# Kernel optimization log

Measured on AMD Instinct MI355X. Metric: run time of the kernel, lower is better.

The kernel has to match this reference:

```python
import jax, jax.numpy as jnp
import numpy as np

N_NODES = 100000
N_EDGES = 1_600_000
N_ROIS = 400
HIDDEN = 128
N_GRAPHS = 512
OUT = 2


def setup_inputs() -> dict:
    key = jax.random.key(0)
    ks = jax.random.split(key, 7)
    x = jax.random.normal(ks[0], (N_NODES, N_ROIS), dtype=jnp.float32)
    edge_index = jax.random.randint(ks[1], (2, N_EDGES), 0, N_NODES, dtype=jnp.int32)
    # sorted graph-assignment vector; prepend arange so every graph id is non-empty
    rnd = jax.random.randint(ks[2], (N_NODES - N_GRAPHS,), 0, N_GRAPHS, dtype=jnp.int32)
    batch = jnp.sort(jnp.concatenate([jnp.arange(N_GRAPHS, dtype=jnp.int32), rnd]))
    W = jax.random.normal(ks[3], (N_ROIS, HIDDEN), dtype=jnp.float32) / np.float32(np.sqrt(N_ROIS))
    b = jnp.zeros((HIDDEN,), dtype=jnp.float32)
    lin_W = jax.random.normal(ks[4], (HIDDEN, OUT), dtype=jnp.float32) / np.float32(np.sqrt(HIDDEN))
    lin_b = jnp.zeros((OUT,), dtype=jnp.float32)
    return {"x": x, "edge_index": edge_index, "batch": batch,
            "W": W, "b": b, "lin_W": lin_W, "lin_b": lin_b}


def reference(x, edge_index, batch, W, b, lin_W, lin_b):
    N = x.shape[0]
    # GCNConv: add self-loops, symmetric normalization D^-1/2 (A+I) D^-1/2
    loops = jnp.arange(N, dtype=edge_index.dtype)
    row = jnp.concatenate([edge_index[0], loops])  # source
    col = jnp.concatenate([edge_index[1], loops])  # target
    deg = jax.ops.segment_sum(jnp.ones_like(col, dtype=x.dtype), col, num_segments=N)
    dinv = jnp.where(deg > 0, jax.lax.rsqrt(deg), 0.0)
    norm = dinv[row] * dinv[col]                   # [E+N]
    h = x @ W                                      # [N, H] transform before propagate
    msg = h[row] * norm[:, None]                   # [E+N, H]
    agg = jax.ops.segment_sum(msg, col, num_segments=N) + b
    act = jax.nn.relu(agg)                         # [N, H]
    # global max pool over graph ids (all segments guaranteed non-empty)
    pooled = jax.ops.segment_max(act, batch, num_segments=N_GRAPHS)  # [G, H]
    logits = pooled @ lin_W + lin_b                # [G, OUT]
    return logits, pooled
```

## Files before the change

kernel.cpp:

```cpp
#include <hip/hip_runtime.h>
#include <hip/hip_bf16.h>

#define N_NODES 100000
#define N_EDGES 1600000
#define N_ROIS  400
#define RKP     416
#define HID     128
#define N_GRAPHS 512
#define NOUT    2
#define NBUCK   391
#define BCAP    8192
#define ECH     4096
#define NPW     16

typedef __attribute__((ext_vector_type(8))) short short8;
typedef __attribute__((ext_vector_type(4))) float f32x4;

static __device__ __forceinline__ unsigned short f2bf(float f) {
  unsigned u = __float_as_uint(f);
  u += 0x7fffu + ((u >> 16) & 1u);
  return (unsigned short)(u >> 16);
}
static __device__ __forceinline__ float bf2f(unsigned short h) {
  return __uint_as_float(((unsigned)h) << 16);
}

__global__ __launch_bounds__(256) void bucket_k(
    const int* __restrict__ row, const int* __restrict__ col,
    int* __restrict__ bcnt, unsigned int* __restrict__ pairs) {
  __shared__ int hist[NBUCK];
  __shared__ int base[NBUCK];
  int t = threadIdx.x;
  for (int b = t; b < NBUCK; b += 256) hist[b] = 0;
  __syncthreads();
  int e0 = blockIdx.x * ECH;
  unsigned int pk[16];
  int bk[16], rk[16];
#pragma unroll
  for (int i = 0; i < 16; ++i) {
    int e = e0 + t + i * 256;
    if (e < N_EDGES) {
      int r = row[e], c = col[e];
      bk[i] = c >> 8;
      pk[i] = ((unsigned)r << 8) | (unsigned)(c & 255);
      rk[i] = atomicAdd(&hist[bk[i]], 1);
    } else bk[i] = -1;
  }
  __syncthreads();
  for (int b = t; b < NBUCK; b += 256)
    base[b] = (hist[b] > 0) ? atomicAdd(&bcnt[b], hist[b]) : 0;
  __syncthreads();
#pragma unroll
  for (int i = 0; i < 16; ++i)
    if (bk[i] >= 0) {
      int p = base[bk[i]] + rk[i];
      if (p < BCAP) pairs[(size_t)bk[i] * BCAP + p] = pk[i];
    }
}

__global__ __launch_bounds__(256) void csr_build_k(
    const unsigned int* __restrict__ pairs, const int* __restrict__ bcnt,
    int* __restrict__ csr_row, int* __restrict__ offs, int* __restrict__ cnt,
    float* __restrict__ dinv) {
  __shared__ unsigned int ep[BCAP];
  __shared__ int h[256];
  __shared__ int sc[256];
  __shared__ int cur[256];
  int b = blockIdx.x;
  int t = threadIdx.x;
  int m = min(bcnt[b], BCAP);
  size_t base = (size_t)b * BCAP;
  for (int j = t; j < m; j += 256) ep[j] = pairs[base + j];
  h[t] = 0;
  __syncthreads();
  for (int j = t; j < m; j += 256) atomicAdd(&h[ep[j] & 255u], 1);
  __syncthreads();
  int myc = h[t];
  sc[t] = myc;
  __syncthreads();
  for (int off = 1; off < 256; off <<= 1) {
    int v = (t >= off) ? sc[t - off] : 0;
    __syncthreads();
    sc[t] += v;
    __syncthreads();
  }
  int loff = sc[t] - myc;
  cur[t] = loff;
  int node = b * 256 + t;
  if (node < N_NODES) {
    cnt[node] = myc;
    offs[node] = (int)base + loff;
    dinv[node] = rsqrtf((float)(myc + 1));
  }
  __syncthreads();
  for (int j = t; j < m; j += 256) {
    unsigned int e = ep[j];
    int pos = atomicAdd(&cur[e & 255u], 1);
    csr_row[base + pos] = (int)(e >> 8);
  }
}

__global__ void prep_wt_k(const float* __restrict__ W, unsigned short* __restrict__ Wt) {
  int idx = blockIdx.x * blockDim.x + threadIdx.x;
  if (idx < HID * RKP) {
    int n = idx / RKP, k = idx - n * RKP;
    float v = (k < N_ROIS) ? W[k * HID + n] : 0.f;
    Wt[idx] = f2bf(v);
  }
}

__global__ __launch_bounds__(256) void gemm_k(
    const float* __restrict__ x, const unsigned short* __restrict__ Wt,
    const float* __restrict__ dinv, unsigned short* __restrict__ hp) {
  __shared__ __align__(16) short As[64][40];
  __shared__ __align__(16) short Bs[HID][40];
  int t = threadIdx.x;
  int lane = t & 63;
  int wv = t >> 6;
  int row0 = blockIdx.x * 64;
  int mrow = lane & 15;
  int kgrp = lane >> 4;

  f32x4 acc[8];
#pragma unroll
  for (int i = 0; i < 8; ++i) acc[i] = (f32x4){0.f, 0.f, 0.f, 0.f};

  int arow = t >> 2;
  int akofs = (t & 3) * 8;
  int brow = t >> 1;
  int bkofs = (t & 1) * 16;
  int grow_a = row0 + arow;
  const float* xp = x + (size_t)grow_a * N_ROIS;

  for (int kk = 0; kk < RKP; kk += 32) {
    short8 a8;
    if (grow_a < N_NODES && kk + akofs + 8 <= N_ROIS) {
      float4 f0 = *(const float4*)(xp + kk + akofs);
      float4 f1 = *(const float4*)(xp + kk + akofs + 4);
      a8[0] = (short)f2bf(f0.x); a8[1] = (short)f2bf(f0.y);
      a8[2] = (short)f2bf(f0.z); a8[3] = (short)f2bf(f0.w);
      a8[4] = (short)f2bf(f1.x); a8[5] = (short)f2bf(f1.y);
      a8[6] = (short)f2bf(f1.z); a8[7] = (short)f2bf(f1.w);
    } else {
#pragma unroll
      for (int u = 0; u < 8; ++u) {
        int k = kk + akofs + u;
        float f = (grow_a < N_NODES && k < N_ROIS) ? xp[k] : 0.f;
        a8[u] = (short)f2bf(f);
      }
    }
    *(short8*)&As[arow][akofs] = a8;
    const short8* wp = (const short8*)(Wt + (size_t)brow * RKP + kk + bkofs);
    *(short8*)&Bs[brow][bkofs] = wp[0];
    *(short8*)&Bs[brow][bkofs + 8] = wp[1];
    __syncthreads();

    short8 af = *(const short8*)&As[wv * 16 + mrow][kgrp * 8];
#pragma unroll
    for (int nt = 0; nt < 8; ++nt) {
      short8 bf = *(const short8*)&Bs[nt * 16 + mrow][kgrp * 8];
      acc[nt] = __builtin_amdgcn_mfma_f32_16x16x32_bf16(af, bf, acc[nt], 0, 0, 0);
    }
    __syncthreads();
  }

#pragma unroll
  for (int r = 0; r < 4; ++r) {
    int grow = row0 + wv * 16 + kgrp * 4 + r;
    if (grow < N_NODES) {
      float di = dinv[grow];
      unsigned short* op = hp + (size_t)grow * HID + mrow;
#pragma unroll
      for (int nt = 0; nt < 8; ++nt) {
        op[nt * 16] = f2bf(di * acc[nt][r]);
      }
    }
  }
}

__global__ __launch_bounds__(256) void gather_k(
    const unsigned short* __restrict__ hp, const int* __restrict__ csr_row,
    const int* __restrict__ offs, const int* __restrict__ cnt,
    const float* __restrict__ dinv, const int* __restrict__ batch,
    const float* __restrict__ bias, unsigned int* __restrict__ pooled_bits) {
  int wave = (blockIdx.x * blockDim.x + threadIdx.x) >> 6;
  int lane = threadIdx.x & 63;
  int n0 = wave * NPW;
  if (n0 >= N_NODES) return;
  int nend = min(n0 + NPW, N_NODES);
  float2 bb = *(const float2*)(bias + lane * 2);
  float rm0 = 0.f, rm1 = 0.f;
  int cur_g = batch[n0];

  for (int i = n0; i < nend; ++i) {
    int start = offs[i];
    int m = cnt[i];
    unsigned int u = *(const unsigned int*)(hp + (size_t)i * HID + lane * 2);
    float ax = bf2f((unsigned short)(u & 0xffff));
    float ay = bf2f((unsigned short)(u >> 16));
    int j = 0;
    for (; j + 4 <= m; j += 4) {
      int s0 = csr_row[start + j];
      int s1 = csr_row[start + j + 1];
      int s2 = csr_row[start + j + 2];
      int s3 = csr_row[start + j + 3];
      unsigned int u0 = *(const unsigned int*)(hp + (size_t)s0 * HID + lane * 2);
      unsigned int u1 = *(const unsigned int*)(hp + (size_t)s1 * HID + lane * 2);
      unsigned int u2 = *(const unsigned int*)(hp + (size_t)s2 * HID + lane * 2);
      unsigned int u3 = *(const unsigned int*)(hp + (size_t)s3 * HID + lane * 2);
      ax += (bf2f((unsigned short)(u0 & 0xffff)) + bf2f((unsigned short)(u1 & 0xffff)))
          + (bf2f((unsigned short)(u2 & 0xffff)) + bf2f((unsigned short)(u3 & 0xffff)));
      ay += (bf2f((unsigned short)(u0 >> 16)) + bf2f((unsigned short)(u1 >> 16)))
          + (bf2f((unsigned short)(u2 >> 16)) + bf2f((unsigned short)(u3 >> 16)));
    }
    for (; j < m; ++j) {
      int s0 = csr_row[start + j];
      unsigned int u0 = *(const unsigned int*)(hp + (size_t)s0 * HID + lane * 2);
      ax += bf2f((unsigned short)(u0 & 0xffff));
      ay += bf2f((unsigned short)(u0 >> 16));
    }
    float di = dinv[i];
    float p0 = fmaxf(fmaf(di, ax, bb.x), 0.f);
    float p1 = fmaxf(fmaf(di, ay, bb.y), 0.f);
    int g = batch[i];
    if (g != cur_g) {
      atomicMax(&pooled_bits[cur_g * HID + lane * 2],     __float_as_uint(rm0));
      atomicMax(&pooled_bits[cur_g * HID + lane * 2 + 1], __float_as_uint(rm1));
      rm0 = 0.f; rm1 = 0.f;
      cur_g = g;
    }
    rm0 = fmaxf(rm0, p0);
    rm1 = fmaxf(rm1, p1);
  }
  atomicMax(&pooled_bits[cur_g * HID + lane * 2],     __float_as_uint(rm0));
  atomicMax(&pooled_bits[cur_g * HID + lane * 2 + 1], __float_as_uint(rm1));
}

__global__ void logits_k(const float* __restrict__ pooled, const float* __restrict__ lin_W,
                         const float* __restrict__ lin_b, float* __restrict__ out) {
  int t = blockIdx.x * blockDim.x + threadIdx.x;
  if (t < N_GRAPHS * NOUT) {
    int g = t >> 1, o = t & 1;
    float s = lin_b[o];
    const float* pg = pooled + g * HID;
#pragma unroll 8
    for (int k = 0; k < HID; ++k) s = fmaf(pg[k], lin_W[k * NOUT + o], s);
    out[t] = s;
  }
}

extern "C" void kernel_launch(void* const* d_in, const int* in_sizes, int n_in,
                              void* d_out, int out_size, void* d_ws, size_t ws_size,
                              hipStream_t stream) {
  (void)in_sizes; (void)n_in; (void)ws_size;
  const float* x     = (const float*)d_in[0];
  const int*   ei    = (const int*)d_in[1];
  const int*   row   = ei;
  const int*   col   = ei + N_EDGES;
  const int*   batch = (const int*)d_in[2];
  const float* W     = (const float*)d_in[3];
  const float* b     = (const float*)d_in[4];
  const float* lin_W = (const float*)d_in[5];
  const float* lin_b = (const float*)d_in[6];
  float* out = (float*)d_out;

  char* ws = (char*)d_ws;
  int*   bcnt    = (int*)(ws + 0);
  int*   offs    = (int*)(ws + 4096);
  int*   cnt     = (int*)(ws + 404096);
  float* dinv    = (float*)(ws + 804096);
  unsigned short* Wt = (unsigned short*)(ws + 1204096);
  int*   csr_row = (int*)(ws + 1310720);
  unsigned int* pairs = (unsigned int*)(ws + 14123008);
  unsigned short* hp  = (unsigned short*)(ws + 14123008);

  hipMemsetAsync(bcnt, 0, NBUCK * sizeof(int), stream);
  hipMemsetAsync(d_out, 0, (size_t)out_size * sizeof(float), stream);

  bucket_k<<<(N_EDGES + ECH - 1) / ECH, 256, 0, stream>>>(row, col, bcnt, pairs);
  csr_build_k<<<NBUCK, 256, 0, stream>>>(pairs, bcnt, csr_row, offs, cnt, dinv);
  prep_wt_k<<<(HID * RKP + 255) / 256, 256, 0, stream>>>(W, Wt);
  gemm_k<<<(N_NODES + 63) / 64, 256, 0, stream>>>(x, Wt, dinv, hp);
  {
    int waves = (N_NODES + NPW - 1) / NPW;
    int blocks = (waves * 64 + 255) / 256;
    gather_k<<<blocks, 256, 0, stream>>>(
        hp, csr_row, offs, cnt, dinv, batch, b,
        (unsigned int*)(out + N_GRAPHS * NOUT));
  }
  logits_k<<<(N_GRAPHS * NOUT + 255) / 256, 256, 0, stream>>>(
      out + N_GRAPHS * NOUT, lin_W, lin_b, out);
}
```

Before: 391.9 us.

## Prepack W into MFMA fragment order, load A directly, widen gather loads

Weights are prepacked into per-lane MFMA fragment order and copied into LDS with global_load_lds in two halves. The GEMM now uses 512-thread blocks that read x straight into registers, which removes the A-tile LDS staging and the per-k-step barriers. The gather kernel splits each wave into four groups that each fetch 16-byte slices of a different neighbour row, combining the partial sums with cross-lane shuffles. CSR segments are padded to multiples of four so neighbour indices can be read as int4, but this changes the offsets and adds a bounds guard that can drop writes near bucket capacity.

```diff
diff --git a/kernel.cpp b/kernel.cpp
--- a/kernel.cpp
+++ b/kernel.cpp
@@ -23,6 +23,12 @@
 }
 static __device__ __forceinline__ float bf2f(unsigned short h) {
   return __uint_as_float(((unsigned)h) << 16);
+}
+
+static __device__ __forceinline__ void gload_lds16(const unsigned short* g, short* l) {
+  __builtin_amdgcn_global_load_lds(
+      (const __attribute__((address_space(1))) void*)g,
+      (__attribute__((address_space(3))) void*)l, 16, 0, 0);
 }
 
 __global__ __launch_bounds__(256) void bucket_k(
@@ -76,7 +82,8 @@
   for (int j = t; j < m; j += 256) atomicAdd(&h[ep[j] & 255u], 1);
   __syncthreads();
   int myc = h[t];
-  sc[t] = myc;
+  int mycp = (myc + 3) & ~3;
+  sc[t] = mycp;
   __syncthreads();
   for (int off = 1; off < 256; off <<= 1) {
     int v = (t >= off) ? sc[t - off] : 0;
@@ -84,7 +91,7 @@
     sc[t] += v;
     __syncthreads();
   }
-  int loff = sc[t] - myc;
+  int loff = sc[t] - mycp;
   cur[t] = loff;
   int node = b * 256 + t;
   if (node < N_NODES) {
@@ -96,47 +103,53 @@
   for (int j = t; j < m; j += 256) {
     unsigned int e = ep[j];
     int pos = atomicAdd(&cur[e & 255u], 1);
-    csr_row[base + pos] = (int)(e >> 8);
-  }
-}
-
-__global__ void prep_wt_k(const float* __restrict__ W, unsigned short* __restrict__ Wt) {
+    if (pos < BCAP) csr_row[base + pos] = (int)(e >> 8);
+  }
+}
+
+__global__ void prep_wt_k(const float* __restrict__ W, unsigned short* __restrict__ Wf) {
   int idx = blockIdx.x * blockDim.x + threadIdx.x;
-  if (idx < HID * RKP) {
-    int n = idx / RKP, k = idx - n * RKP;
-    float v = (k < N_ROIS) ? W[k * HID + n] : 0.f;
-    Wt[idx] = f2bf(v);
-  }
-}
-
-__global__ __launch_bounds__(256) void gemm_k(
-    const float* __restrict__ x, const unsigned short* __restrict__ Wt,
+  if (idx >= 13 * 8 * 64 * 8) return;
+  int u    = idx & 7;
+  int lane = (idx >> 3) & 63;
+  int nt   = (idx >> 9) & 7;
+  int kk5  = idx >> 12;
+  int n = nt * 16 + (lane & 15);
+  int k = kk5 * 32 + (lane >> 4) * 8 + u;
+  Wf[idx] = (k < N_ROIS) ? f2bf(W[k * HID + n]) : (unsigned short)0;
+}
+
+__global__ __launch_bounds__(512, 4) void gemm_k(
+    const float* __restrict__ x, const unsigned short* __restrict__ Wf,
     const float* __restrict__ dinv, unsigned short* __restrict__ hp) {
-  __shared__ __align__(16) short As[64][40];
-  __shared__ __align__(16) short Bs[HID][40];
+  __shared__ __align__(16) short Bs[28672];
   int t = threadIdx.x;
-  int lane = t & 63;
-  int wv = t >> 6;
-  int row0 = blockIdx.x * 64;
-  int mrow = lane & 15;
-  int kgrp = lane >> 4;
+  int lane = t & 63, wv = t >> 6;
+  int mrow = lane & 15, kg = lane >> 4;
+  int row0 = blockIdx.x * 128;
+  int arow = row0 + wv * 16 + mrow;
+  bool rowok = arow < N_NODES;
+  const float* xp = x + (size_t)arow * N_ROIS;
 
   f32x4 acc[8];
 #pragma unroll
   for (int i = 0; i < 8; ++i) acc[i] = (f32x4){0.f, 0.f, 0.f, 0.f};
 
-  int arow = t >> 2;
-  int akofs = (t & 3) * 8;
-  int brow = t >> 1;
-  int bkofs = (t & 1) * 16;
-  int grow_a = row0 + arow;
-  const float* xp = x + (size_t)grow_a * N_ROIS;
-
-  for (int kk = 0; kk < RKP; kk += 32) {
+#pragma unroll
+  for (int c = 0; c < 7; ++c) {
+    int ch = wv * 7 + c;
+    gload_lds16(Wf + (size_t)ch * 512 + lane * 8, &Bs[ch * 512]);
+  }
+  asm volatile("s_waitcnt vmcnt(0)" ::: "memory");
+  __syncthreads();
+
+#pragma unroll
+  for (int kf = 0; kf < 7; ++kf) {
+    int k0 = kf * 32 + kg * 8;
     short8 a8;
-    if (grow_a < N_NODES && kk + akofs + 8 <= N_ROIS) {
-      float4 f0 = *(const float4*)(xp + kk + akofs);
-      float4 f1 = *(const float4*)(xp + kk + akofs + 4);
+    if (rowok && k0 + 8 <= N_ROIS) {
+      float4 f0 = *(const float4*)(xp + k0);
+      float4 f1 = *(const float4*)(xp + k0 + 4);
       a8[0] = (short)f2bf(f0.x); a8[1] = (short)f2bf(f0.y);
       a8[2] = (short)f2bf(f0.z); a8[3] = (short)f2bf(f0.w);
       a8[4] = (short)f2bf(f1.x); a8[5] = (short)f2bf(f1.y);
@@ -144,38 +157,74 @@
     } else {
 #pragma unroll
       for (int u = 0; u < 8; ++u) {
-        int k = kk + akofs + u;
-        float f = (grow_a < N_NODES && k < N_ROIS) ? xp[k] : 0.f;
+        int k = k0 + u;
+        float f = (rowok && k < N_ROIS) ? xp[k] : 0.f;
         a8[u] = (short)f2bf(f);
       }
     }
-    *(short8*)&As[arow][akofs] = a8;
-    const short8* wp = (const short8*)(Wt + (size_t)brow * RKP + kk + bkofs);
-    *(short8*)&Bs[brow][bkofs] = wp[0];
-    *(short8*)&Bs[brow][bkofs + 8] = wp[1];
-    __syncthreads();
-
-    short8 af = *(const short8*)&As[wv * 16 + mrow][kgrp * 8];
 #pragma unroll
     for (int nt = 0; nt < 8; ++nt) {
-      short8 bf = *(const short8*)&Bs[nt * 16 + mrow][kgrp * 8];
-      acc[nt] = __builtin_amdgcn_mfma_f32_16x16x32_bf16(af, bf, acc[nt], 0, 0, 0);
-    }
-    __syncthreads();
+      short8 bf = *(const short8*)&Bs[(kf * 8 + nt) * 512 + lane * 8];
+      acc[nt] = __builtin_amdgcn_mfma_f32_16x16x32_bf16(a8, bf, acc[nt], 0, 0, 0);
+    }
+  }
+  __syncthreads();
+
+#pragma unroll
+  for (int c = 0; c < 6; ++c) {
+    int ch = wv * 6 + c;
+    gload_lds16(Wf + (size_t)(56 + ch) * 512 + lane * 8, &Bs[ch * 512]);
+  }
+  asm volatile("s_waitcnt vmcnt(0)" ::: "memory");
+  __syncthreads();
+
+#pragma unroll
+  for (int kf = 0; kf < 6; ++kf) {
+    int k0 = (kf + 7) * 32 + kg * 8;
+    short8 a8;
+    if (rowok && k0 + 8 <= N_ROIS) {
+      float4 f0 = *(const float4*)(xp + k0);
+      float4 f1 = *(const float4*)(xp + k0 + 4);
+      a8[0] = (short)f2bf(f0.x); a8[1] = (short)f2bf(f0.y);
+      a8[2] = (short)f2bf(f0.z); a8[3] = (short)f2bf(f0.w);
+      a8[4] = (short)f2bf(f1.x); a8[5] = (short)f2bf(f1.y);
+      a8[6] = (short)f2bf(f1.z); a8[7] = (short)f2bf(f1.w);
+    } else {
+#pragma unroll
+      for (int u = 0; u < 8; ++u) {
+        int k = k0 + u;
+        float f = (rowok && k < N_ROIS) ? xp[k] : 0.f;
+        a8[u] = (short)f2bf(f);
+      }
+    }
+#pragma unroll
+    for (int nt = 0; nt < 8; ++nt) {
+      short8 bf = *(const short8*)&Bs[(kf * 8 + nt) * 512 + lane * 8];
+      acc[nt] = __builtin_amdgcn_mfma_f32_16x16x32_bf16(a8, bf, acc[nt], 0, 0, 0);
+    }
   }
 
 #pragma unroll
   for (int r = 0; r < 4; ++r) {
-    int grow = row0 + wv * 16 + kgrp * 4 + r;
+    int grow = row0 + wv * 16 + kg * 4 + r;
     if (grow < N_NODES) {
       float di = dinv[grow];
       unsigned short* op = hp + (size_t)grow * HID + mrow;
 #pragma unroll
-      for (int nt = 0; nt < 8; ++nt) {
-        op[nt * 16] = f2bf(di * acc[nt][r]);
-      }
-    }
-  }
+      for (int nt = 0; nt < 8; ++nt) op[nt * 16] = f2bf(di * acc[nt][r]);
+    }
+  }
+}
+
+static __device__ __forceinline__ void acc8(float* a, uint4 u) {
+  a[0] += bf2f((unsigned short)(u.x));
+  a[1] += bf2f((unsigned short)(u.x >> 16));
+  a[2] += bf2f((unsigned short)(u.y));
+  a[3] += bf2f((unsigned short)(u.y >> 16));
+  a[4] += bf2f((unsigned short)(u.z));
+  a[5] += bf2f((unsigned short)(u.z >> 16));
+  a[6] += bf2f((unsigned short)(u.w));
+  a[7] += bf2f((unsigned short)(u.w >> 16));
 }
 
 __global__ __launch_bounds__(256) void gather_k(
@@ -185,55 +234,67 @@
     const float* __restrict__ bias, unsigned int* __restrict__ pooled_bits) {
   int wave = (blockIdx.x * blockDim.x + threadIdx.x) >> 6;
   int lane = threadIdx.x & 63;
+  int g  = lane >> 4;
+  int cg = lane & 15;
   int n0 = wave * NPW;
   if (n0 >= N_NODES) return;
   int nend = min(n0 + NPW, N_NODES);
-  float2 bb = *(const float2*)(bias + lane * 2);
-  float rm0 = 0.f, rm1 = 0.f;
+  float bv[8];
+  {
+    float4 b0 = *(const float4*)(bias + cg * 8);
+    float4 b1 = *(const float4*)(bias + cg * 8 + 4);
+    bv[0] = b0.x; bv[1] = b0.y; bv[2] = b0.z; bv[3] = b0.w;
+    bv[4] = b1.x; bv[5] = b1.y; bv[6] = b1.z; bv[7] = b1.w;
+  }
+  float rm[8];
+#pragma unroll
+  for (int k = 0; k < 8; ++k) rm[k] = 0.f;
   int cur_g = batch[n0];
 
   for (int i = n0; i < nend; ++i) {
     int start = offs[i];
     int m = cnt[i];
-    unsigned int u = *(const unsigned int*)(hp + (size_t)i * HID + lane * 2);
-    float ax = bf2f((unsigned short)(u & 0xffff));
-    float ay = bf2f((unsigned short)(u >> 16));
-    int j = 0;
-    for (; j + 4 <= m; j += 4) {
-      int s0 = csr_row[start + j];
-      int s1 = csr_row[start + j + 1];
-      int s2 = csr_row[start + j + 2];
-      int s3 = csr_row[start + j + 3];
-      unsigned int u0 = *(const unsigned int*)(hp + (size_t)s0 * HID + lane * 2);
-      unsigned int u1 = *(const unsigned int*)(hp + (size_t)s1 * HID + lane * 2);
-      unsigned int u2 = *(const unsigned int*)(hp + (size_t)s2 * HID + lane * 2);
-      unsigned int u3 = *(const unsigned int*)(hp + (size_t)s3 * HID + lane * 2);
-      ax += (bf2f((unsigned short)(u0 & 0xffff)) + bf2f((unsigned short)(u1 & 0xffff)))
-          + (bf2f((unsigned short)(u2 & 0xffff)) + bf2f((unsigned short)(u3 & 0xffff)));
-      ay += (bf2f((unsigned short)(u0 >> 16)) + bf2f((unsigned short)(u1 >> 16)))
-          + (bf2f((unsigned short)(u2 >> 16)) + bf2f((unsigned short)(u3 >> 16)));
-    }
-    for (; j < m; ++j) {
-      int s0 = csr_row[start + j];
-      unsigned int u0 = *(const unsigned int*)(hp + (size_t)s0 * HID + lane * 2);
-      ax += bf2f((unsigned short)(u0 & 0xffff));
-      ay += bf2f((unsigned short)(u0 >> 16));
+    float a[8];
+#pragma unroll
+    for (int k = 0; k < 8; ++k) a[k] = 0.f;
+    if (g == 0) {
+      uint4 u = *(const uint4*)(hp + (size_t)i * HID + cg * 8);
+      acc8(a, u);
+    }
+    for (int j = 0; j < m; j += 4) {
+      int4 q = *(const int4*)(csr_row + start + j);
+      int s = (g == 0) ? q.x : (g == 1) ? q.y : (g == 2) ? q.z : q.w;
+      if (j + g < m) {
+        uint4 u = *(const uint4*)(hp + (size_t)s * HID + cg * 8);
+        acc8(a, u);
+      }
+    }
+#pragma unroll
+    for (int k = 0; k < 8; ++k) {
+      a[k] += __shfl_xor(a[k], 16);
+      a[k] += __shfl_xor(a[k], 32);
     }
     float di = dinv[i];
-    float p0 = fmaxf(fmaf(di, ax, bb.x), 0.f);
-    float p1 = fmaxf(fmaf(di, ay, bb.y), 0.f);
-    int g = batch[i];
-    if (g != cur_g) {
-      atomicMax(&pooled_bits[cur_g * HID + lane * 2],     __float_as_uint(rm0));
-      atomicMax(&pooled_bits[cur_g * HID + lane * 2 + 1], __float_as_uint(rm1));
-      rm0 = 0.f; rm1 = 0.f;
-      cur_g = g;
-    }
-    rm0 = fmaxf(rm0, p0);
-    rm1 = fmaxf(rm1, p1);
-  }
-  atomicMax(&pooled_bits[cur_g * HID + lane * 2],     __float_as_uint(rm0));
-  atomicMax(&pooled_bits[cur_g * HID + lane * 2 + 1], __float_as_uint(rm1));
+    int gb = batch[i];
+    if (gb != cur_g) {
+      if (lane < 16) {
+#pragma unroll
+        for (int k = 0; k < 8; ++k)
+          atomicMax(&pooled_bits[cur_g * HID + cg * 8 + k], __float_as_uint(rm[k]));
+      }
+#pragma unroll
+      for (int k = 0; k < 8; ++k) rm[k] = 0.f;
+      cur_g = gb;
+    }
+#pragma unroll
+    for (int k = 0; k < 8; ++k)
+      rm[k] = fmaxf(rm[k], fmaxf(fmaf(di, a[k], bv[k]), 0.f));
+  }
+  if (lane < 16) {
+#pragma unroll
+    for (int k = 0; k < 8; ++k)
+      atomicMax(&pooled_bits[cur_g * HID + cg * 8 + k], __float_as_uint(rm[k]));
+  }
 }
 
 __global__ void logits_k(const float* __restrict__ pooled, const float* __restrict__ lin_W,
@@ -269,7 +330,7 @@
   int*   offs    = (int*)(ws + 4096);
   int*   cnt     = (int*)(ws + 404096);
   float* dinv    = (float*)(ws + 804096);
-  unsigned short* Wt = (unsigned short*)(ws + 1204096);
+  unsigned short* Wf = (unsigned short*)(ws + 1204096);
   int*   csr_row = (int*)(ws + 1310720);
   unsigned int* pairs = (unsigned int*)(ws + 14123008);
   unsigned short* hp  = (unsigned short*)(ws + 14123008);
@@ -279,8 +340,8 @@
 
   bucket_k<<<(N_EDGES + ECH - 1) / ECH, 256, 0, stream>>>(row, col, bcnt, pairs);
   csr_build_k<<<NBUCK, 256, 0, stream>>>(pairs, bcnt, csr_row, offs, cnt, dinv);
-  prep_wt_k<<<(HID * RKP + 255) / 256, 256, 0, stream>>>(W, Wt);
-  gemm_k<<<(N_NODES + 63) / 64, 256, 0, stream>>>(x, Wt, dinv, hp);
+  prep_wt_k<<<(13 * 8 * 64 * 8 + 255) / 256, 256, 0, stream>>>(W, Wf);
+  gemm_k<<<(N_NODES + 127) / 128, 512, 0, stream>>>(x, Wf, dinv, hp);
   {
     int waves = (N_NODES + NPW - 1) / NPW;
     int blocks = (waves * 64 + 255) / 256;
```

Measured after the change: 395.6 us. About the same (+1.0%).
